# Kernel optimization log

Hardware: AMD Instinct MI355X
Metric: run time of the kernel (lower is better)

## Reference

```python
import jax, jax.numpy as jnp
import numpy as np

D_MODEL = 768
NUM_HEADS = 12
HEAD_DIM = D_MODEL // NUM_HEADS  # 64, also rotary dim
INTERMEDIATE = 1152
WINDOW = 128          # config.local_attention (layer_id=1 -> local layer)
ROPE_BASE = 10000.0   # local_rope_theta
EPS = 1e-5


def layer_norm_nocenter(x, gamma):
    # keras LayerNormalization(center=False): mean-subtract, no beta
    mu = jnp.mean(x, axis=-1, keepdims=True)
    var = jnp.var(x, axis=-1, keepdims=True)
    return (x - mu) * jax.lax.rsqrt(var + EPS) * gamma


def rotate_half(x):
    x1, x2 = jnp.split(x, 2, axis=-1)
    return jnp.concatenate([-x2, x1], axis=-1)


def setup_inputs() -> dict:
    key = jax.random.key(0)
    ks = jax.random.split(key, 7)
    B, S = 4, 2048
    hidden_states = jax.random.normal(ks[0], (B, S, D_MODEL), dtype=jnp.float32)
    attention_mask = jnp.zeros((B, 1, S, S), dtype=jnp.float32)  # no padding
    s = 0.02
    attn_norm_gamma = jnp.ones((D_MODEL,), dtype=jnp.float32)
    wqkv = jax.random.normal(ks[1], (D_MODEL, 3 * D_MODEL), dtype=jnp.float32) * s
    wo_attn = jax.random.normal(ks[2], (D_MODEL, D_MODEL), dtype=jnp.float32) * s
    mlp_norm_gamma = jnp.ones((D_MODEL,), dtype=jnp.float32)
    wi = jax.random.normal(ks[3], (D_MODEL, 2 * INTERMEDIATE), dtype=jnp.float32) * s
    wo_mlp = jax.random.normal(ks[4], (INTERMEDIATE, D_MODEL), dtype=jnp.float32) * s
    return {
        'hidden_states': hidden_states,
        'attention_mask': attention_mask,
        'attn_norm_gamma': attn_norm_gamma,
        'wqkv': wqkv,
        'wo_attn': wo_attn,
        'mlp_norm_gamma': mlp_norm_gamma,
        'wi': wi,
        'wo_mlp': wo_mlp,
    }


def reference(hidden_states, attention_mask, attn_norm_gamma, wqkv, wo_attn,
              mlp_norm_gamma, wi, wo_mlp):
    B, S, Dm = hidden_states.shape
    H, Dh = NUM_HEADS, HEAD_DIM

    # RoPE cache (NTKScaling with scaling_factor=1 -> plain RoPE)
    idx = jnp.arange(0, Dh, 2, dtype=jnp.float32)
    inv_freq = 1.0 / (ROPE_BASE ** (idx / Dh))          # [Dh/2]
    t = jnp.arange(S, dtype=jnp.float32)
    freqs = t[:, None] * inv_freq[None, :]              # [S, Dh/2]
    emb = jnp.concatenate([freqs, freqs], axis=-1)      # [S, Dh]
    cos = jnp.cos(emb)[None, None]                      # [1,1,S,Dh]
    sin = jnp.sin(emb)[None, None]

    # combined sliding-window + padding mask
    pos = jnp.arange(S)
    dist = jnp.abs(pos[:, None] - pos[None, :])
    neg = jnp.finfo(jnp.float32).min
    local = jnp.where(dist <= WINDOW // 2, 0.0, neg).astype(jnp.float32)
    mask = attention_mask + local[None, None]           # [B,1,S,S]

    # attention (layer_id != 0 -> pre-norm)
    x = layer_norm_nocenter(hidden_states, attn_norm_gamma)
    qkv = (x @ wqkv).reshape(B, S, 3, H, Dh).transpose(2, 0, 3, 1, 4)
    q, k, v = qkv[0], qkv[1], qkv[2]                    # [B,H,S,Dh]
    q = q * cos + rotate_half(q) * sin
    k = k * cos + rotate_half(k) * sin

    scale = 1.0 / jnp.sqrt(jnp.asarray(Dh, q.dtype))
    scores = jnp.einsum('bhqd,bhkd->bhqk', q, k) * scale + mask
    attn = jax.nn.softmax(scores, axis=-1)
    ctx = jnp.einsum('bhqk,bhkd->bhqd', attn, v)
    attn_out = ctx.transpose(0, 2, 1, 3).reshape(B, S, Dm) @ wo_attn

    h = hidden_states + attn_out

    # GLU MLP: Wi -> split -> gelu(x)*gate -> Wo, residual
    n = layer_norm_nocenter(h, mlp_norm_gamma)
    x_in, gate = jnp.split(n @ wi, 2, axis=-1)
    mlp = jax.nn.gelu(x_in, approximate=False) * gate
    return h + mlp @ wo_mlp
```

## Files before the change

kernel.cpp:

```cpp
#include <hip/hip_runtime.h>
#include <cstdint>
#include <cstddef>

typedef __bf16 bf16;
typedef float f32x4 __attribute__((ext_vector_type(4)));
typedef __bf16 bf16x8 __attribute__((ext_vector_type(8)));
typedef __bf16 bf16x4 __attribute__((ext_vector_type(4)));
typedef __bf16 bf16x2 __attribute__((ext_vector_type(2)));

#define MFMA16(a, b, c) __builtin_amdgcn_mfma_f32_16x16x32_bf16((a), (b), (c), 0, 0, 0)

__device__ __forceinline__ void gload_lds16(const void* g, void* l) {
  __builtin_amdgcn_global_load_lds((__attribute__((address_space(1))) void*)g,
                                   (__attribute__((address_space(3))) void*)l,
                                   16, 0, 0);
}

__global__ __launch_bounds__(256) void wconv_ln(const float* __restrict__ wqkv,
                                                const float* __restrict__ woa,
                                                const float* __restrict__ wi,
                                                const float* __restrict__ wom,
                                                bf16* __restrict__ wqkvT,
                                                bf16* __restrict__ woaT,
                                                bf16* __restrict__ wiT,
                                                bf16* __restrict__ womT,
                                                const float* __restrict__ X,
                                                const float* __restrict__ gamma,
                                                bf16* __restrict__ xnout) {
  __shared__ float tile[32][33];
  const int t = threadIdx.x;
  int id = blockIdx.x;
  if (id >= 4896) {
    const int row = id - 4896;
    const float* xr = X + (size_t)row * 768;
    float v0 = xr[t], v1 = xr[t + 256], v2 = xr[t + 512];
    float s = v0 + v1 + v2;
    float s2 = v0 * v0 + v1 * v1 + v2 * v2;
#pragma unroll
    for (int m = 1; m <= 32; m <<= 1) {
      s += __shfl_xor(s, m, 64);
      s2 += __shfl_xor(s2, m, 64);
    }
    float* red = &tile[0][0];
    const int w = t >> 6, lane = t & 63;
    if (lane == 0) { red[w] = s; red[4 + w] = s2; }
    __syncthreads();
    s = red[0] + red[1] + red[2] + red[3];
    s2 = red[4] + red[5] + red[6] + red[7];
    const float mu = s * (1.f / 768.f);
    const float var = s2 * (1.f / 768.f) - mu * mu;
    const float rs = rsqrtf(var + 1e-5f);
    xnout[(size_t)row * 768 + t] = (bf16)((v0 - mu) * rs * gamma[t]);
    xnout[(size_t)row * 768 + t + 256] = (bf16)((v1 - mu) * rs * gamma[t + 256]);
    xnout[(size_t)row * 768 + t + 512] = (bf16)((v2 - mu) * rs * gamma[t + 512]);
    return;
  }
  const float* W;
  bf16* Wt;
  int K, N, bx, by;
  if (id < 1728) { W = wqkv; Wt = wqkvT; K = 768; N = 2304; bx = id % 72; by = id / 72; }
  else if (id < 2304) { id -= 1728; W = woa; Wt = woaT; K = 768; N = 768; bx = id % 24; by = id / 24; }
  else if (id < 4032) { id -= 2304; W = wi; Wt = wiT; K = 768; N = 2304; bx = id % 72; by = id / 72; }
  else { id -= 4032; W = wom; Wt = womT; K = 1152; N = 768; bx = id % 24; by = id / 24; }
  const int n0 = bx * 32, k0 = by * 32;
  const int c = t & 31, r = t >> 5;
#pragma unroll
  for (int i = 0; i < 4; ++i)
    tile[r + i * 8][c] = W[(size_t)(k0 + r + i * 8) * N + n0 + c];
  __syncthreads();
#pragma unroll
  for (int i = 0; i < 4; ++i)
    Wt[(size_t)(n0 + r + i * 8) * K + k0 + c] = (bf16)tile[c][r + i * 8];
}

__global__ __launch_bounds__(256) void ln_kernel(const float* __restrict__ X,
                                                 const float* __restrict__ gamma,
                                                 bf16* __restrict__ out) {
  const int row = blockIdx.x, t = threadIdx.x;
  const float* xr = X + (size_t)row * 768;
  float v0 = xr[t], v1 = xr[t + 256], v2 = xr[t + 512];
  float s = v0 + v1 + v2;
  float s2 = v0 * v0 + v1 * v1 + v2 * v2;
#pragma unroll
  for (int m = 1; m <= 32; m <<= 1) {
    s += __shfl_xor(s, m, 64);
    s2 += __shfl_xor(s2, m, 64);
  }
  __shared__ float red[8];
  const int w = t >> 6, lane = t & 63;
  if (lane == 0) { red[w] = s; red[4 + w] = s2; }
  __syncthreads();
  s = red[0] + red[1] + red[2] + red[3];
  s2 = red[4] + red[5] + red[6] + red[7];
  const float mu = s * (1.f / 768.f);
  const float var = s2 * (1.f / 768.f) - mu * mu;
  const float rs = rsqrtf(var + 1e-5f);
  out[(size_t)row * 768 + t] = (bf16)((v0 - mu) * rs * gamma[t]);
  out[(size_t)row * 768 + t + 256] = (bf16)((v1 - mu) * rs * gamma[t + 256]);
  out[(size_t)row * 768 + t + 512] = (bf16)((v2 - mu) * rs * gamma[t + 512]);
}

#define GEMM_CORE_LOOP(NT_, AROW_EXPR, BROW_EXPR)                                   \
  auto stage = [&](int tile) {                                                      \
    const int kk0 = tile * 64;                                                      \
    bf16* Ab_ = &SM[(tile & 1) * 24576];                                            \
    bf16* Bb_ = Ab_ + 16384;                                                        \
    _Pragma("unroll") for (int i = 0; i < 4; ++i) {                                 \
      int c = i * 512 + t;                                                          \
      int r = c >> 3, j = (c & 7) ^ (r & 7);                                        \
      gload_lds16(Ap + (size_t)(AROW_EXPR) * Kd + (kk0 + j * 8), &Ab_[c * 8]);      \
    }                                                                               \
    _Pragma("unroll") for (int i = 0; i < 2; ++i) {                                 \
      int c = i * 512 + t;                                                          \
      int r = c >> 3, j = (c & 7) ^ (r & 7);                                        \
      gload_lds16(Bp + (size_t)(BROW_EXPR) * Kd + (kk0 + j * 8), &Bb_[c * 8]);      \
    }                                                                               \
  };                                                                                \
  stage(0);                                                                         \
  stage(1);                                                                         \
  asm volatile("s_waitcnt vmcnt(6)" ::: "memory");                                  \
  __builtin_amdgcn_s_barrier();                                                     \
  __builtin_amdgcn_sched_barrier(0);                                                \
  for (int tt = 0; tt < NT_; ++tt) {                                                \
    const bf16* Ab = &SM[(tt & 1) * 24576];                                         \
    const bf16* Bb = Ab + 16384;                                                    \
    bf16x8 af[4], bfr[4];                                                           \
                                                                \
    _Pragma("unroll") for (int mt = 0; mt < 4; ++mt) {                              \
      int r = wm * 64 + mt * 16 + rm;                                               \
      af[mt] = *(const bf16x8*)&Ab[r * 64 + ((qd ^ (r & 7)) * 8)];                  \
    }                                                                               \
    _Pragma("unroll") for (int nt = 0; nt < 4; ++nt) {                              \
      int r = wn * 64 + nt * 16 + rm;                                               \
      bfr[nt] = *(const bf16x8*)&Bb[r * 64 + ((qd ^ (r & 7)) * 8)];                 \
    }                                                                               \
    __builtin_amdgcn_s_barrier();                                                   \
    __builtin_amdgcn_sched_barrier(0);                                              \
    __builtin_amdgcn_s_setprio(1);                                                  \
    _Pragma("unroll") for (int mt = 0; mt < 4; ++mt)                                \
        _Pragma("unroll") for (int nt = 0; nt < 4; ++nt)                            \
            acc[mt][nt] = MFMA16(af[mt], bfr[nt], acc[mt][nt]);                     \
    __builtin_amdgcn_s_setprio(0);                                                  \
    __builtin_amdgcn_s_barrier();                                                   \
    __builtin_amdgcn_sched_barrier(0);                                              \
                                                                \
    _Pragma("unroll") for (int mt = 0; mt < 4; ++mt) {                              \
      int r = wm * 64 + mt * 16 + rm;                                               \
      af[mt] = *(const bf16x8*)&Ab[r * 64 + (((4 + qd) ^ (r & 7)) * 8)];            \
    }                                                                               \
    _Pragma("unroll") for (int nt = 0; nt < 4; ++nt) {                              \
      int r = wn * 64 + nt * 16 + rm;                                               \
      bfr[nt] = *(const bf16x8*)&Bb[r * 64 + (((4 + qd) ^ (r & 7)) * 8)];           \
    }                                                                               \
    asm volatile("s_waitcnt lgkmcnt(0)" ::: "memory");                              \
    __builtin_amdgcn_sched_barrier(0);                                              \
    __builtin_amdgcn_s_barrier();           \
    __builtin_amdgcn_sched_barrier(0);                                              \
    if (tt + 2 < NT_) stage(tt + 2);                                                \
    __builtin_amdgcn_s_setprio(1);                                                  \
    _Pragma("unroll") for (int mt = 0; mt < 4; ++mt)                                \
        _Pragma("unroll") for (int nt = 0; nt < 4; ++nt)                            \
            acc[mt][nt] = MFMA16(af[mt], bfr[nt], acc[mt][nt]);                     \
    __builtin_amdgcn_s_setprio(0);                                                  \
    if (tt + 2 < NT_) {                                                             \
      asm volatile("s_waitcnt vmcnt(6)" ::: "memory");                              \
    } else {                                                                        \
      asm volatile("s_waitcnt vmcnt(0)" ::: "memory");                              \
    }                                                                               \
    __builtin_amdgcn_s_barrier();                                                   \
    __builtin_amdgcn_sched_barrier(0);                                              \
  }

template <int EPI, int NT>
__global__ __launch_bounds__(512, 2) void gemm_big(const bf16* __restrict__ Ap,
                                                   const bf16* __restrict__ Bp,
                                                   const float* __restrict__ Res,
                                                   void* __restrict__ Cout,
                                                   int Nout) {
  constexpr int Kd = NT * 64;
  __shared__ __align__(16) bf16 SM[49152];
  const int t = threadIdx.x;
  const int lane = t & 63, w = t >> 6;
  const int wm = w >> 1, wn = w & 1;
  const int rm = lane & 15, qd = lane >> 4;
  const int by = blockIdx.y;
  const int row0 = blockIdx.x * 256;
  f32x4 acc[4][4] = {};

  auto brow = [&](int r) -> int {
    if constexpr (EPI == 1) {
      int q = (r >> 4) & 3;
      return ((q & 1) ? 1152 : 0) + by * 64 + (r >> 6) * 32 + ((q >> 1) << 4) + (r & 15);
    } else {
      return by * 128 + r;
    }
  };

  GEMM_CORE_LOOP(NT, row0 + r, brow(r))

  if constexpr (EPI == 0) {
    float* C = (float*)Cout;
#pragma unroll
    for (int mt = 0; mt < 4; ++mt)
#pragma unroll
      for (int nt = 0; nt < 4; ++nt) {
        const int gc = by * 128 + wn * 64 + nt * 16 + rm;
#pragma unroll
        for (int r = 0; r < 4; ++r) {
          const int gr = row0 + wm * 64 + mt * 16 + qd * 4 + r;
          const size_t idx = (size_t)gr * Nout + gc;
          C[idx] = Res[idx] + acc[mt][nt][r];
        }
      }
  } else {
    bf16* C = (bf16*)Cout;
#pragma unroll
    for (int mt = 0; mt < 4; ++mt)
#pragma unroll
      for (int g = 0; g < 2; ++g) {
        const int gc = by * 64 + wn * 32 + g * 16 + rm;
#pragma unroll
        for (int r = 0; r < 4; ++r) {
          const int gr = row0 + wm * 64 + mt * 16 + qd * 4 + r;
          const float x = acc[mt][g * 2][r], gv = acc[mt][g * 2 + 1][r];
          const float ge = 0.5f * x * (1.0f + erff(x * 0.70710678118654752f));
          C[(size_t)gr * 1152 + gc] = (bf16)(ge * gv);
        }
      }
  }
}

__global__ __launch_bounds__(512, 2) void gemm_qkv2(const bf16* __restrict__ Ap,
                                                    const bf16* __restrict__ Bp,
                                                    bf16* __restrict__ Qb,
                                                    bf16* __restrict__ Kb,
                                                    bf16* __restrict__ Vt) {
  constexpr int Kd = 768;
  __shared__ __align__(16) bf16 SM[49152];
  const int t = threadIdx.x;
  const int lane = t & 63, w = t >> 6;
  const int wm = w >> 1, wn = w & 1;
  const int rm = lane & 15, qd = lane >> 4;
  const int by = blockIdx.y;
  const int row0 = blockIdx.x * 256;
  f32x4 acc[4][4] = {};

  GEMM_CORE_LOOP(12, row0 + r, by * 128 + r)

  const int head_id = by * 2 + wn;
  const int typ = by / 6;
  const int b = row0 >> 11;
  const int sblk = row0 & 2047;
  const int sw = sblk + wm * 64;

  if (typ < 2) {
    const int h = head_id - typ * 12;
    const size_t bhbase = (size_t)(b * 12 + h) * 2048;
    bf16* dst = typ ? Kb : Qb;
    constexpr float inv2pi = 0.15915494309189535f;
#pragma unroll
    for (int nt = 0; nt < 2; ++nt) {
      const int d = nt * 16 + rm;
      const float invf = exp2f((float)d * -0.41524101186092029f);
      float rev = (float)(sw + qd * 4) * invf * inv2pi;
      rev -= floorf(rev);
      float cs = __builtin_amdgcn_cosf(rev);
      float sn = __builtin_amdgcn_sinf(rev);
      float rv1 = invf * inv2pi;
      float c1 = __builtin_amdgcn_cosf(rv1), s1 = __builtin_amdgcn_sinf(rv1);
      float rv13 = 13.f * invf * inv2pi;
      rv13 -= floorf(rv13);
      float c13 = __builtin_amdgcn_cosf(rv13), s13 = __builtin_amdgcn_sinf(rv13);
#pragma unroll
      for (int mt = 0; mt < 4; ++mt)
#pragma unroll
        for (int r = 0; r < 4; ++r) {
          const int s = sw + mt * 16 + qd * 4 + r;
          const float x1 = acc[mt][nt][r], x2 = acc[mt][nt + 2][r];
          bf16x2 v2;
          v2[0] = (bf16)(x1 * cs - x2 * sn);
          v2[1] = (bf16)(x2 * cs + x1 * sn);
          *(bf16x2*)&dst[(bhbase + s) * 64 + 2 * d] = v2;
          const float ca = (r < 3) ? c1 : c13, sa = (r < 3) ? s1 : s13;
          const float cn = cs * ca - sn * sa;
          sn = sn * ca + cs * sa;
          cs = cn;
        }
    }
  } else {
#pragma unroll
    for (int mt = 0; mt < 4; ++mt)
#pragma unroll
      for (int nt = 0; nt < 4; ++nt) {
        int hd = wn * 64 + nt * 16 + rm;
        int sl = wm * 64 + mt * 16 + qd * 4;
        bf16x4 v4;
#pragma unroll
        for (int r = 0; r < 4; ++r) v4[r] = (bf16)acc[mt][nt][r];
        *(bf16x4*)&SM[hd * 264 + sl] = v4;
      }
    __syncthreads();
    const int h0 = by * 2 - 24;
#pragma unroll
    for (int it = 0; it < 8; ++it) {
      int cc = it * 512 + t;
      int hd = cc >> 5, s8 = (cc & 31) * 8;
      bf16x8 vv = *(const bf16x8*)&SM[hd * 264 + s8];
      size_t grow = (size_t)(b * 12 + h0 + (hd >> 6)) * 64 + (hd & 63);
      *(bf16x8*)&Vt[grow * 2048 + sblk + s8] = vv;
    }
  }
}

__global__ __launch_bounds__(256) void attn_kernel(const bf16* __restrict__ Qb,
                                                   const bf16* __restrict__ Kb,
                                                   const bf16* __restrict__ Vt,
                                                   const float* __restrict__ am,
                                                   bf16* __restrict__ ctx) {
  __shared__ __align__(16) bf16 KP[64 * 200];
  __shared__ __align__(16) bf16 Vts[64 * 192];
  bf16* Ks = KP;
  bf16* Ps = KP;

  const int t = threadIdx.x;
  const int lane = t & 63, w = t >> 6;
  const int rm = lane & 15, qd = lane >> 4;
  const int s0 = blockIdx.x * 64;
  const int bh = blockIdx.y;
  const int b = bh / 12, h = bh - b * 12;
  const size_t baseQ = (size_t)bh * 2048;

#pragma unroll
  for (int i = 0; i < 6; ++i) {
    int c = i * 256 + t;
    int r = c >> 3, j = (c & 7) ^ (r & 7);
    int key = min(max(s0 - 64 + r, 0), 2047);
    gload_lds16(Kb + (baseQ + key) * 64 + j * 8, &Ks[c * 8]);
  }
#pragma unroll
  for (int i = 0; i < 6; ++i) {
    int c = i * 256 + t;
    int r = c / 24, jl = c - r * 24;
    int j = (jl & 24) | ((jl & 7) ^ (r & 7));
    int k0 = min(max(s0 - 64 + j * 8, 0), 2040);
    gload_lds16(Vt + ((size_t)bh * 64 + r) * 2048 + k0, &Vts[c * 8]);
  }

  bf16x8 aq[2];
#pragma unroll
  for (int kb = 0; kb < 2; ++kb)
    aq[kb] = *(const bf16x8*)&Qb[(baseQ + s0 + w * 16 + rm) * 64 + kb * 32 + qd * 8];

  float msk[12][4];
#pragma unroll
  for (int nt = 0; nt < 12; ++nt) {
    int key = s0 - 64 + nt * 16 + rm;
#pragma unroll
    for (int r = 0; r < 4; ++r) {
      int qpos = s0 + w * 16 + qd * 4 + r;
      bool valid = (key >= 0) && (key < 2048) && (key - qpos <= 64) && (qpos - key <= 64);
      msk[nt][r] = valid ? am[((size_t)b * 2048 + qpos) * 2048 + key] : -3e38f;
    }
  }
  __syncthreads();

  f32x4 sc[12];
#pragma unroll
  for (int nt = 0; nt < 12; ++nt) {
    f32x4 a = {0.f, 0.f, 0.f, 0.f};
#pragma unroll
    for (int kb = 0; kb < 2; ++kb) {
      int r = nt * 16 + rm;
      bf16x8 bk = *(const bf16x8*)&Ks[r * 64 + (((kb * 4 + qd) ^ (rm & 7)) * 8)];
      a = MFMA16(aq[kb], bk, a);
    }
    sc[nt] = a;
  }

  float mx[4] = {-3e38f, -3e38f, -3e38f, -3e38f};
#pragma unroll
  for (int nt = 0; nt < 12; ++nt)
#pragma unroll
    for (int r = 0; r < 4; ++r) {
      float v = (msk[nt][r] <= -2.9e38f) ? -3e38f : sc[nt][r] * 0.125f + msk[nt][r];
      sc[nt][r] = v;
      mx[r] = fmaxf(mx[r], v);
    }
#pragma unroll
  for (int r = 0; r < 4; ++r)
#pragma unroll
    for (int m = 1; m <= 8; m <<= 1) mx[r] = fmaxf(mx[r], __shfl_xor(mx[r], m, 64));
  float sum[4] = {0.f, 0.f, 0.f, 0.f};
#pragma unroll
  for (int nt = 0; nt < 12; ++nt)
#pragma unroll
    for (int r = 0; r < 4; ++r) {
      float p = (sc[nt][r] > -1e37f) ? __expf(sc[nt][r] - mx[r]) : 0.f;
      sc[nt][r] = p;
      sum[r] += p;
    }
#pragma unroll
  for (int r = 0; r < 4; ++r)
#pragma unroll
    for (int m = 1; m <= 8; m <<= 1) sum[r] += __shfl_xor(sum[r], m, 64);
  float inv[4];
#pragma unroll
  for (int r = 0; r < 4; ++r) inv[r] = 1.f / sum[r];

  __syncthreads();

#pragma unroll
  for (int nt = 0; nt < 12; ++nt)
#pragma unroll
    for (int r = 0; r < 4; ++r)
      Ps[(w * 16 + qd * 4 + r) * 200 + nt * 16 + rm] = (bf16)(sc[nt][r] * inv[r]);

  f32x4 o[4] = {};
#pragma unroll
  for (int ks = 0; ks < 6; ++ks) {
    bf16x8 ap = *(const bf16x8*)&Ps[(w * 16 + rm) * 200 + ks * 32 + qd * 8];
#pragma unroll
    for (int nt = 0; nt < 4; ++nt) {
      int kc = ks * 4 + qd;
      bf16x8 bv = *(const bf16x8*)&Vts[(nt * 16 + rm) * 192 +
                                       (((kc & 24) | ((kc & 7) ^ (rm & 7))) * 8)];
      o[nt] = MFMA16(ap, bv, o[nt]);
    }
  }
#pragma unroll
  for (int nt = 0; nt < 4; ++nt)
#pragma unroll
    for (int r = 0; r < 4; ++r) {
      int q_ = s0 + w * 16 + qd * 4 + r;
      ctx[((size_t)(b * 2048 + q_)) * 768 + h * 64 + nt * 16 + rm] = (bf16)o[nt][r];
    }
}

extern "C" void kernel_launch(void* const* d_in, const int* in_sizes, int n_in,
                              void* d_out, int out_size, void* d_ws, size_t ws_size,
                              hipStream_t stream) {
  (void)in_sizes; (void)n_in; (void)out_size; (void)ws_size;
  const float* hidden = (const float*)d_in[0];
  const float* amask = (const float*)d_in[1];
  const float* g1 = (const float*)d_in[2];
  const float* wqkv = (const float*)d_in[3];
  const float* woa = (const float*)d_in[4];
  const float* g2 = (const float*)d_in[5];
  const float* wi = (const float*)d_in[6];
  const float* wom = (const float*)d_in[7];
  float* out = (float*)d_out;

  char* p = (char*)d_ws;
  size_t o = 0;
  auto take = [&](size_t bytes) {
    char* r = p + o;
    o = (o + bytes + 255) & ~(size_t)255;
    return r;
  };
  bf16* wqkvT = (bf16*)take((size_t)2304 * 768 * 2);
  bf16* woaT = (bf16*)take((size_t)768 * 768 * 2);
  bf16* wiT = (bf16*)take((size_t)2304 * 768 * 2);
  bf16* womT = (bf16*)take((size_t)768 * 1152 * 2);
  bf16* xn = (bf16*)take((size_t)8192 * 768 * 2);
  bf16* Qb = (bf16*)take((size_t)98304 * 64 * 2);
  bf16* Kb = (bf16*)take((size_t)98304 * 64 * 2);
  bf16* Vt = (bf16*)take((size_t)98304 * 64 * 2);
  bf16* ctxb = (bf16*)take((size_t)8192 * 768 * 2);
  float* hbuf = (float*)take((size_t)8192 * 768 * 4);
  bf16* mlp = (bf16*)take((size_t)8192 * 1152 * 2);

  wconv_ln<<<13088, 256, 0, stream>>>(wqkv, woa, wi, wom, wqkvT, woaT, wiT, womT,
                                      hidden, g1, xn);

  gemm_qkv2<<<dim3(32, 18), 512, 0, stream>>>(xn, wqkvT, Qb, Kb, Vt);
  attn_kernel<<<dim3(32, 48), 256, 0, stream>>>(Qb, Kb, Vt, amask, ctxb);
  gemm_big<0, 12><<<dim3(32, 6), 512, 0, stream>>>(ctxb, woaT, hidden, hbuf, 768);

  ln_kernel<<<8192, 256, 0, stream>>>(hbuf, g2, xn);
  gemm_big<1, 12><<<dim3(32, 18), 512, 0, stream>>>(xn, wiT, nullptr, mlp, 1152);
  gemm_big<0, 18><<<dim3(32, 6), 512, 0, stream>>>(mlp, womT, hbuf, out, 768);
}
```

Baseline: 307.8 us.

## Triple-buffer GEMM LDS stages, split prefetch into halves, swap attention grid order

The shared GEMM main loop moves from double to triple LDS buffering (48K to 72K bf16 elements per block). Each tile prefetch is split into two halves, issued alongside the two MFMA sub-phases, so global-to-LDS copies overlap compute and the trailing barrier wait is shorter. The attention launch grid is transposed so consecutive blocks cover different heads at the same sequence tile, which changes cache locality. The larger LDS footprint (144KB per block) may prevent two blocks per CU despite the launch bounds. The vmcnt(6) wait count was not adjusted for the new 3-loads-per-half issue pattern, which could risk correctness or ordering.

```diff
diff --git a/kernel.cpp b/kernel.cpp
--- a/kernel.cpp
+++ b/kernel.cpp
@@ -101,31 +101,31 @@
 }
 
 #define GEMM_CORE_LOOP(NT_, AROW_EXPR, BROW_EXPR)                                   \
-  auto stage = [&](int tile) {                                                      \
+  auto stage = [&](int tile, int half) {                                            \
     const int kk0 = tile * 64;                                                      \
-    bf16* Ab_ = &SM[(tile & 1) * 24576];                                            \
+    bf16* Ab_ = &SM[(tile % 3) * 24576];                                            \
     bf16* Bb_ = Ab_ + 16384;                                                        \
-    _Pragma("unroll") for (int i = 0; i < 4; ++i) {                                 \
-      int c = i * 512 + t;                                                          \
+    _Pragma("unroll") for (int i = 0; i < 2; ++i) {                                 \
+      int c = (half * 2 + i) * 512 + t;                                             \
       int r = c >> 3, j = (c & 7) ^ (r & 7);                                        \
       gload_lds16(Ap + (size_t)(AROW_EXPR) * Kd + (kk0 + j * 8), &Ab_[c * 8]);      \
     }                                                                               \
-    _Pragma("unroll") for (int i = 0; i < 2; ++i) {                                 \
-      int c = i * 512 + t;                                                          \
+    {                                                                               \
+      int c = half * 512 + t;                                                       \
       int r = c >> 3, j = (c & 7) ^ (r & 7);                                        \
       gload_lds16(Bp + (size_t)(BROW_EXPR) * Kd + (kk0 + j * 8), &Bb_[c * 8]);      \
     }                                                                               \
   };                                                                                \
-  stage(0);                                                                         \
-  stage(1);                                                                         \
+  stage(0, 0); stage(0, 1);                                                         \
+  stage(1, 0); stage(1, 1);                                                         \
   asm volatile("s_waitcnt vmcnt(6)" ::: "memory");                                  \
   __builtin_amdgcn_s_barrier();                                                     \
   __builtin_amdgcn_sched_barrier(0);                                                \
   for (int tt = 0; tt < NT_; ++tt) {                                                \
-    const bf16* Ab = &SM[(tt & 1) * 24576];                                         \
+    const bf16* Ab = &SM[(tt % 3) * 24576];                                         \
     const bf16* Bb = Ab + 16384;                                                    \
     bf16x8 af[4], bfr[4];                                                           \
-                                                                \
+                                                           \
     _Pragma("unroll") for (int mt = 0; mt < 4; ++mt) {                              \
       int r = wm * 64 + mt * 16 + rm;                                               \
       af[mt] = *(const bf16x8*)&Ab[r * 64 + ((qd ^ (r & 7)) * 8)];                  \
@@ -134,16 +134,19 @@
       int r = wn * 64 + nt * 16 + rm;                                               \
       bfr[nt] = *(const bf16x8*)&Bb[r * 64 + ((qd ^ (r & 7)) * 8)];                 \
     }                                                                               \
+    if (tt + 2 < NT_) stage(tt + 2, 0);                                             \
     __builtin_amdgcn_s_barrier();                                                   \
+    __builtin_amdgcn_sched_barrier(0);                                              \
+    asm volatile("s_waitcnt lgkmcnt(0)" ::: "memory");                              \
     __builtin_amdgcn_sched_barrier(0);                                              \
     __builtin_amdgcn_s_setprio(1);                                                  \
     _Pragma("unroll") for (int mt = 0; mt < 4; ++mt)                                \
-        _Pragma("unroll") for (int nt = 0; nt < 4; ++nt)                            \
-            acc[mt][nt] = MFMA16(af[mt], bfr[nt], acc[mt][nt]);                     \
+      _Pragma("unroll") for (int nt = 0; nt < 4; ++nt)                              \
+        acc[mt][nt] = MFMA16(af[mt], bfr[nt], acc[mt][nt]);                         \
     __builtin_amdgcn_s_setprio(0);                                                  \
     __builtin_amdgcn_s_barrier();                                                   \
     __builtin_amdgcn_sched_barrier(0);                                              \
-                                                                \
+                                                           \
     _Pragma("unroll") for (int mt = 0; mt < 4; ++mt) {                              \
       int r = wm * 64 + mt * 16 + rm;                                               \
       af[mt] = *(const bf16x8*)&Ab[r * 64 + (((4 + qd) ^ (r & 7)) * 8)];            \
@@ -152,33 +155,30 @@
       int r = wn * 64 + nt * 16 + rm;                                               \
       bfr[nt] = *(const bf16x8*)&Bb[r * 64 + (((4 + qd) ^ (r & 7)) * 8)];           \
     }                                                                               \
+    if (tt + 2 < NT_) stage(tt + 2, 1);                                             \
+    __builtin_amdgcn_s_barrier();                                                   \
+    __builtin_amdgcn_sched_barrier(0);                                              \
     asm volatile("s_waitcnt lgkmcnt(0)" ::: "memory");                              \
     __builtin_amdgcn_sched_barrier(0);                                              \
-    __builtin_amdgcn_s_barrier();           \
-    __builtin_amdgcn_sched_barrier(0);                                              \
-    if (tt + 2 < NT_) stage(tt + 2);                                                \
     __builtin_amdgcn_s_setprio(1);                                                  \
     _Pragma("unroll") for (int mt = 0; mt < 4; ++mt)                                \
-        _Pragma("unroll") for (int nt = 0; nt < 4; ++nt)                            \
-            acc[mt][nt] = MFMA16(af[mt], bfr[nt], acc[mt][nt]);                     \
+      _Pragma("unroll") for (int nt = 0; nt < 4; ++nt)                              \
+        acc[mt][nt] = MFMA16(af[mt], bfr[nt], acc[mt][nt]);                         \
     __builtin_amdgcn_s_setprio(0);                                                  \
-    if (tt + 2 < NT_) {                                                             \
-      asm volatile("s_waitcnt vmcnt(6)" ::: "memory");                              \
-    } else {                                                                        \
-      asm volatile("s_waitcnt vmcnt(0)" ::: "memory");                              \
-    }                                                                               \
+    if (tt + 2 < NT_) { asm volatile("s_waitcnt vmcnt(6)" ::: "memory"); }          \
+    else if (tt + 1 < NT_) { asm volatile("s_waitcnt vmcnt(0)" ::: "memory"); }     \
     __builtin_amdgcn_s_barrier();                                                   \
     __builtin_amdgcn_sched_barrier(0);                                              \
   }
 
 template <int EPI, int NT>
-__global__ __launch_bounds__(512, 2) void gemm_big(const bf16* __restrict__ Ap,
-                                                   const bf16* __restrict__ Bp,
-                                                   const float* __restrict__ Res,
-                                                   void* __restrict__ Cout,
-                                                   int Nout) {
+__global__ __launch_bounds__(512, 2) void gemm_pipe(const bf16* __restrict__ Ap,
+                                                    const bf16* __restrict__ Bp,
+                                                    const float* __restrict__ Res,
+                                                    void* __restrict__ Cout,
+                                                    int Nout) {
   constexpr int Kd = NT * 64;
-  __shared__ __align__(16) bf16 SM[49152];
+  __shared__ __align__(16) bf16 SM[73728];
   const int t = threadIdx.x;
   const int lane = t & 63, w = t >> 6;
   const int wm = w >> 1, wn = w & 1;
@@ -230,13 +230,13 @@
   }
 }
 
-__global__ __launch_bounds__(512, 2) void gemm_qkv2(const bf16* __restrict__ Ap,
+__global__ __launch_bounds__(512, 2) void gemm_qkv3(const bf16* __restrict__ Ap,
                                                     const bf16* __restrict__ Bp,
                                                     bf16* __restrict__ Qb,
                                                     bf16* __restrict__ Kb,
                                                     bf16* __restrict__ Vt) {
   constexpr int Kd = 768;
-  __shared__ __align__(16) bf16 SM[49152];
+  __shared__ __align__(16) bf16 SM[73728];
   const int t = threadIdx.x;
   const int lane = t & 63, w = t >> 6;
   const int wm = w >> 1, wn = w & 1;
@@ -325,8 +325,8 @@
   const int t = threadIdx.x;
   const int lane = t & 63, w = t >> 6;
   const int rm = lane & 15, qd = lane >> 4;
-  const int s0 = blockIdx.x * 64;
-  const int bh = blockIdx.y;
+  const int s0 = blockIdx.y * 64;
+  const int bh = blockIdx.x;
   const int b = bh / 12, h = bh - b * 12;
   const size_t baseQ = (size_t)bh * 2048;
 
@@ -472,11 +472,11 @@
   wconv_ln<<<13088, 256, 0, stream>>>(wqkv, woa, wi, wom, wqkvT, woaT, wiT, womT,
                                       hidden, g1, xn);
 
-  gemm_qkv2<<<dim3(32, 18), 512, 0, stream>>>(xn, wqkvT, Qb, Kb, Vt);
-  attn_kernel<<<dim3(32, 48), 256, 0, stream>>>(Qb, Kb, Vt, amask, ctxb);
-  gemm_big<0, 12><<<dim3(32, 6), 512, 0, stream>>>(ctxb, woaT, hidden, hbuf, 768);
+  gemm_qkv3<<<dim3(32, 18), 512, 0, stream>>>(xn, wqkvT, Qb, Kb, Vt);
+  attn_kernel<<<dim3(48, 32), 256, 0, stream>>>(Qb, Kb, Vt, amask, ctxb);
+  gemm_pipe<0, 12><<<dim3(32, 6), 512, 0, stream>>>(ctxb, woaT, hidden, hbuf, 768);
 
   ln_kernel<<<8192, 256, 0, stream>>>(hbuf, g2, xn);
-  gemm_big<1, 12><<<dim3(32, 18), 512, 0, stream>>>(xn, wiT, nullptr, mlp, 1152);
-  gemm_big<0, 18><<<dim3(32, 6), 512, 0, stream>>>(mlp, womT, hbuf, out, 768);
-}
+  gemm_pipe<1, 12><<<dim3(32, 18), 512, 0, stream>>>(xn, wiT, nullptr, mlp, 1152);
+  gemm_pipe<0, 18><<<dim3(32, 6), 512, 0, stream>>>(mlp, womT, hbuf, out, 768);
+}
```

After: 292.0 us, median of 3. 5.1% less time.
